# Kernel optimization log

Measured on AMD Instinct MI355X. Metric: run time of the kernel, lower is better.

The kernel has to match this reference:

```python
import jax, jax.numpy as jnp
import numpy as np

D_MODEL = 1024
N_HEADS = 16
D_HEAD = D_MODEL // N_HEADS  # 64
SCALE = 1.0 / float(np.sqrt(D_HEAD))


def setup_inputs() -> dict:
    key = jax.random.key(0)
    kx, kq, kk, kv, ko = jax.random.split(key, 5)
    B, L = 1, 4096
    x = jax.random.normal(kx, (B, L, D_MODEL), dtype=jnp.float32)
    init = 0.02  # small init so softmax isn't saturated
    Wq = jax.random.normal(kq, (D_MODEL, D_MODEL), dtype=jnp.float32) * init
    Wk = jax.random.normal(kk, (D_MODEL, D_MODEL), dtype=jnp.float32) * init
    Wv = jax.random.normal(kv, (D_MODEL, D_MODEL), dtype=jnp.float32) * init
    Wo = jax.random.normal(ko, (D_MODEL, D_MODEL), dtype=jnp.float32) * init
    return {"x": x, "Wq": Wq, "Wk": Wk, "Wv": Wv, "Wo": Wo}


def reference(x, Wq, Wk, Wv, Wo):
    # x: [B, L, d_model]; torch Linear (no bias): y = x @ W.T
    B, L, _ = x.shape

    def split_heads(t):  # [B, L, d_model] -> [B, H, L, Dh]
        return t.reshape(B, L, N_HEADS, D_HEAD).transpose(0, 2, 1, 3)

    q = split_heads(x @ Wq.T)
    k = split_heads(x @ Wk.T)
    v = split_heads(x @ Wv.T)

    # Full (non-flash) attention: explicit [B, H, L, L] scores (causal=False, eval dropout=0)
    scores = jnp.einsum("bhld,bhmd->bhlm", q, k) * SCALE
    attn = jax.nn.softmax(scores, axis=-1)
    out = jnp.einsum("bhlm,bhmd->bhld", attn, v)

    out = out.transpose(0, 2, 1, 3).reshape(B, L, D_MODEL)
    return out @ Wo.T
```

## Files before the change

### kernel.cpp

```cpp
#include <hip/hip_runtime.h>

typedef _Float16 f16_t;
typedef __fp16 fp16x2 __attribute__((ext_vector_type(2)));
typedef _Float16 f16x2 __attribute__((ext_vector_type(2)));
typedef _Float16 f16x4 __attribute__((ext_vector_type(4)));
typedef _Float16 f16x8 __attribute__((ext_vector_type(8)));
typedef float f32x4 __attribute__((ext_vector_type(4)));

#define D_MODEL 1024
#define LSEQ 4096
#define NH 16
#define DH 64
#define QSCALE 0.18033688011112042f

#define GLDS16(g, l)                                                     \
    __builtin_amdgcn_global_load_lds(                                    \
        (const __attribute__((address_space(1))) void*)(g),              \
        (__attribute__((address_space(3))) void*)(l), 16, 0, 0)

#define WAIT_VM(n) asm volatile("s_waitcnt vmcnt(" #n ")" ::: "memory")

__global__ __launch_bounds__(256) void cvt_x(const float* __restrict__ in,
                                             f16_t* __restrict__ out, int n) {
    int i = (blockIdx.x * 256 + threadIdx.x) * 4;
    if (i + 3 < n) {
        float4 v = *(const float4*)&in[i];
        alignas(8) f16_t o4[4] = {(f16_t)v.x, (f16_t)v.y, (f16_t)v.z, (f16_t)v.w};
        *(uint2*)&out[i] = *(const uint2*)o4;
    }
}

__global__ __launch_bounds__(256) void cvt_w4(const float* __restrict__ w0,
                                              const float* __restrict__ w1,
                                              const float* __restrict__ w2,
                                              const float* __restrict__ w3,
                                              f16_t* __restrict__ out) {
    const int q = blockIdx.y;
    const float* src = (q == 0) ? w0 : (q == 1) ? w1 : (q == 2) ? w2 : w3;
    const float scale = (q == 0) ? QSCALE : 1.f;
    int i = (blockIdx.x * 256 + threadIdx.x) * 4;
    float4 v = *(const float4*)&src[i];
    alignas(8) f16_t o4[4] = {(f16_t)(v.x * scale), (f16_t)(v.y * scale),
                              (f16_t)(v.z * scale), (f16_t)(v.w * scale)};
    *(uint2*)&out[(size_t)q * (D_MODEL * D_MODEL) + i] = *(const uint2*)o4;
}

__global__ __launch_bounds__(256, 3) void gemm_f16(const f16_t* __restrict__ A,
                                                   const f16_t* __restrict__ B,
                                                   void* __restrict__ Cout,
                                                   int M, int N, int K, int mode) {
    __shared__ alignas(16) f16_t As[3][128 * 32];
    __shared__ alignas(16) f16_t Bs[3][128 * 32];

    const int tid  = threadIdx.x;
    const int wave = tid >> 6;
    const int lane = tid & 63;
    const int quad = lane >> 4;
    const int l16  = lane & 15;
    const int wm = (wave & 1) * 64;
    const int wn = (wave >> 1) * 64;
    const int bm = blockIdx.x * 128;
    const int bn = blockIdx.y * 128;

    f32x4 acc[4][4] = {};
    const int nk = K / 32;

    auto stage = [&](int kt, int b) {
        const int c0 = wave * 2;
        GLDS16(&A[(size_t)(bm + c0 * 16 + l16) * K + kt * 32 + quad * 8],
               &As[b][c0 * 512]);
        GLDS16(&A[(size_t)(bm + (c0 + 1) * 16 + l16) * K + kt * 32 + quad * 8],
               &As[b][(c0 + 1) * 512]);
        GLDS16(&B[(size_t)(bn + c0 * 16 + l16) * K + kt * 32 + quad * 8],
               &Bs[b][c0 * 512]);
        GLDS16(&B[(size_t)(bn + (c0 + 1) * 16 + l16) * K + kt * 32 + quad * 8],
               &Bs[b][(c0 + 1) * 512]);
    };

    stage(0, 0);
    stage(1, 1);
    for (int kt = 0; kt < nk; ++kt) {
        const int cb = kt % 3;
        if (kt < nk - 1) WAIT_VM(4);
        else             WAIT_VM(0);
        __syncthreads();
        if (kt + 2 < nk) stage(kt + 2, (kt + 2) % 3);

        f16x8 af[4], bfr[4];
#pragma unroll
        for (int mt = 0; mt < 4; ++mt)
            af[mt] = *(const f16x8*)&As[cb][((wm >> 4) + mt) * 512 + lane * 8];
#pragma unroll
        for (int nt = 0; nt < 4; ++nt)
            bfr[nt] = *(const f16x8*)&Bs[cb][((wn >> 4) + nt) * 512 + lane * 8];
#pragma unroll
        for (int mt = 0; mt < 4; ++mt)
#pragma unroll
            for (int nt = 0; nt < 4; ++nt)
                acc[mt][nt] = __builtin_amdgcn_mfma_f32_16x16x32_f16(
                    bfr[nt], af[mt], acc[mt][nt], 0, 0, 0);
    }

#pragma unroll
    for (int mt = 0; mt < 4; ++mt)
#pragma unroll
        for (int nt = 0; nt < 4; ++nt) {
            int row = bm + wm + mt * 16 + l16;
            int col = bn + wn + nt * 16 + quad * 4;
            if (mode == 0) {
                f16x4 p = {(f16_t)acc[mt][nt][0], (f16_t)acc[mt][nt][1],
                           (f16_t)acc[mt][nt][2], (f16_t)acc[mt][nt][3]};
                *(f16x4*)&((f16_t*)Cout)[((size_t)(col >> 6) * M + row) * 64 +
                                         (col & 63)] = p;
            } else {
                *(f32x4*)&((float*)Cout)[(size_t)row * N + col] = acc[mt][nt];
            }
        }
}

__global__ __launch_bounds__(256) void transpose_v(const f16_t* __restrict__ vh,
                                                   f16_t* __restrict__ v4) {
    __shared__ f16_t Ts[64][72];
    const int t = threadIdx.x;
    const int lt = blockIdx.x;
    const int head = blockIdx.y;

#pragma unroll
    for (int i = 0; i < 2; ++i) {
        int idx = t + i * 256;
        int row = idx >> 3, part = idx & 7;
        *(uint4*)&Ts[row][part * 8] =
            *(const uint4*)&vh[((size_t)head * LSEQ + lt * 64 + row) * DH + part * 8];
    }
    __syncthreads();

    const int c   = t >> 4;
    const int dt  = c >> 2, kb = c & 3;
    const int km2 = (t & 15) >> 2;
    const int dl2 = t & 3;
    alignas(16) f16_t buf[16];
#pragma unroll
    for (int i = 0; i < 16; ++i) {
        int j = i & 3, dd = i >> 2;
        buf[i] = Ts[kb * 16 + km2 * 4 + j][dt * 16 + dl2 * 4 + dd];
    }
    f16_t* dst = v4 + (size_t)head * (LSEQ * DH) + lt * 4096 + c * 256 + (t & 15) * 16;
    *(uint4*)&dst[0] = *(const uint4*)&buf[0];
    *(uint4*)&dst[8] = *(const uint4*)&buf[8];
}

__global__ __launch_bounds__(512, 2) void attn_kernel(const f16_t* __restrict__ qh,
                                                      const f16_t* __restrict__ kh,
                                                      const f16_t* __restrict__ v4,
                                                      f16_t* __restrict__ ao) {
    __shared__ alignas(16) f16_t smem[32768];
    __shared__ alignas(16) float lscr[16 * 64];
    f16_t* KsB = smem;
    f16_t* VsB = smem + 16384;

    const int tid  = threadIdx.x;
    const int wave = tid >> 6;
    const int lane = tid & 63;
    const int quad = lane >> 4;
    const int l16  = lane & 15;
    const int wq   = wave & 3;
    const int kha  = wave >> 2;

    const int id = blockIdx.x;
    const int head = id & 15;
    const int qrow0 = (id >> 4) * 256 + wq * 64;

    const f16_t* Q  = qh + (size_t)head * LSEQ * DH;
    const f16_t* K  = kh + (size_t)head * LSEQ * DH;
    const f16_t* V4 = v4 + (size_t)head * (LSEQ * DH);

    f16x8 qf[4][2];
#pragma unroll
    for (int qt = 0; qt < 4; ++qt)
#pragma unroll
        for (int kc = 0; kc < 2; ++kc)
            qf[qt][kc] = *(const f16x8*)
                &Q[(size_t)(qrow0 + qt * 16 + l16) * DH + kc * 32 + quad * 8];

    f32x4 o[4][4] = {};
    float lp[4] = {0.f, 0.f, 0.f, 0.f};

    auto stage = [&](int kt, int b) {
        f16_t* ks = KsB + (kha * 2 + b) * 4096;
        f16_t* vs = VsB + (kha * 2 + b) * 4096;
        const int ktg = kha * 32 + kt;
#pragma unroll
        for (int jj = 0; jj < 2; ++jj) {
            const int j = wq * 2 + jj;
            GLDS16(&K[(size_t)(ktg * 64 + wq * 16 + l16) * DH + jj * 32 + quad * 8],
                   &ks[j * 512]);
            GLDS16(&V4[(size_t)ktg * 4096 + wq * 1024 + jj * 512 + lane * 8],
                   &vs[wq * 1024 + jj * 512]);
        }
    };

    const int NT = LSEQ / 2 / 64;
    stage(0, 0);
    for (int kt = 0; kt < NT; ++kt) {
        const int cb = kt & 1;
        WAIT_VM(0);
        __syncthreads();
        if (kt + 1 < NT) stage(kt + 1, cb ^ 1);

        const f16_t* ks = KsB + (kha * 2 + cb) * 4096;
        const f16_t* vs = VsB + (kha * 2 + cb) * 4096;

#pragma unroll
        for (int mt = 0; mt < 4; ++mt) {
            f16x8 kf0 = *(const f16x8*)&ks[(mt * 2 + 0) * 512 + lane * 8];
            f16x8 kf1 = *(const f16x8*)&ks[(mt * 2 + 1) * 512 + lane * 8];

            f32x4 s[4] = {};
#pragma unroll
            for (int qt = 0; qt < 4; ++qt) {
                s[qt] = __builtin_amdgcn_mfma_f32_16x16x32_f16(kf0, qf[qt][0],
                                                               s[qt], 0, 0, 0);
                s[qt] = __builtin_amdgcn_mfma_f32_16x16x32_f16(kf1, qf[qt][1],
                                                               s[qt], 0, 0, 0);
            }

            f16x4 vfd[4];
#pragma unroll
            for (int dt = 0; dt < 4; ++dt)
                vfd[dt] = *(const f16x4*)&vs[(dt * 4 + mt) * 256 + lane * 4];

#pragma unroll
            for (int qt = 0; qt < 4; ++qt) {
                float e0 = __builtin_amdgcn_exp2f(s[qt][0]);
                float e1 = __builtin_amdgcn_exp2f(s[qt][1]);
                float e2 = __builtin_amdgcn_exp2f(s[qt][2]);
                float e3 = __builtin_amdgcn_exp2f(s[qt][3]);
                lp[qt] += (e0 + e1) + (e2 + e3);
                fp16x2 p01 = __builtin_amdgcn_cvt_pkrtz(e0, e1);
                fp16x2 p23 = __builtin_amdgcn_cvt_pkrtz(e2, e3);
                f16x4 p = {__builtin_bit_cast(f16x2, p01)[0],
                           __builtin_bit_cast(f16x2, p01)[1],
                           __builtin_bit_cast(f16x2, p23)[0],
                           __builtin_bit_cast(f16x2, p23)[1]};
#pragma unroll
                for (int dt = 0; dt < 4; ++dt)
                    o[dt][qt] = __builtin_amdgcn_mfma_f32_16x16x16f16(
                        vfd[dt], p, o[dt][qt], 0, 0, 0);
            }
        }
    }

    __syncthreads();
    float* scr = (float*)smem;
    if (wave >= 4) {
#pragma unroll
        for (int dt = 0; dt < 4; ++dt)
#pragma unroll
            for (int qt = 0; qt < 4; ++qt)
                *(f32x4*)&scr[(((wave - 4) * 16 + dt * 4 + qt) * 64 + lane) * 4] =
                    o[dt][qt];
#pragma unroll
        for (int qt = 0; qt < 4; ++qt)
            lscr[((wave - 4) * 4 + qt) * 64 + lane] = lp[qt];
    }
    __syncthreads();
    if (wave < 4) {
#pragma unroll
        for (int dt = 0; dt < 4; ++dt)
#pragma unroll
            for (int qt = 0; qt < 4; ++qt)
                o[dt][qt] += *(const f32x4*)
                    &scr[((wave * 16 + dt * 4 + qt) * 64 + lane) * 4];
#pragma unroll
        for (int qt = 0; qt < 4; ++qt) {
            float t = lp[qt] + lscr[(wave * 4 + qt) * 64 + lane];
            t += __shfl_xor(t, 16, 64);
            t += __shfl_xor(t, 32, 64);
            lp[qt] = 1.f / t;
        }
#pragma unroll
        for (int dt = 0; dt < 4; ++dt)
#pragma unroll
            for (int qt = 0; qt < 4; ++qt) {
                f16x4 ov = {(f16_t)(o[dt][qt][0] * lp[qt]),
                            (f16_t)(o[dt][qt][1] * lp[qt]),
                            (f16_t)(o[dt][qt][2] * lp[qt]),
                            (f16_t)(o[dt][qt][3] * lp[qt])};
                int qrow = qrow0 + qt * 16 + l16;
                *(f16x4*)&ao[(size_t)qrow * D_MODEL + head * 64 + dt * 16 +
                             quad * 4] = ov;
            }
    }
}

extern "C" void kernel_launch(void* const* d_in, const int* in_sizes, int n_in,
                              void* d_out, int out_size, void* d_ws, size_t ws_size,
                              hipStream_t stream) {
    const float* x  = (const float*)d_in[0];
    const float* Wq = (const float*)d_in[1];
    const float* Wk = (const float*)d_in[2];
    const float* Wv = (const float*)d_in[3];
    const float* Wo = (const float*)d_in[4];

    f16_t* xb = (f16_t*)d_ws;
    f16_t* wq = xb + (size_t)LSEQ * D_MODEL;
    f16_t* wo = wq + (size_t)3 * D_MODEL * D_MODEL;
    f16_t* qh = wo + (size_t)D_MODEL * D_MODEL;
    f16_t* kh = qh + (size_t)LSEQ * D_MODEL;
    f16_t* vh = kh + (size_t)LSEQ * D_MODEL;
    f16_t* v4 = vh + (size_t)LSEQ * D_MODEL;
    f16_t* ao = v4 + (size_t)LSEQ * D_MODEL;

    const int nx = LSEQ * D_MODEL;
    cvt_x<<<nx / 1024, 256, 0, stream>>>(x, xb, nx);
    cvt_w4<<<dim3(D_MODEL * D_MODEL / 1024, 4), 256, 0, stream>>>(Wq, Wk, Wv, Wo, wq);

    gemm_f16<<<dim3(LSEQ / 128, 3 * D_MODEL / 128), 256, 0, stream>>>(
        xb, wq, qh, LSEQ, 3 * D_MODEL, D_MODEL, 0);

    transpose_v<<<dim3(LSEQ / 64, NH), 256, 0, stream>>>(vh, v4);

    attn_kernel<<<dim3((LSEQ / 256) * NH), 512, 0, stream>>>(qh, kh, v4, ao);

    gemm_f16<<<dim3(LSEQ / 128, D_MODEL / 128), 256, 0, stream>>>(
        ao, wo, d_out, LSEQ, D_MODEL, D_MODEL, 1);
}
```

Measured before the change: 259.9 us.

## Use 16x16x32 MFMA for PV product with re-laid-out V tiles

The PV accumulation now pairs two 16-key score tiles and issues a single 16x16x32 f16 MFMA per output tile instead of two 16x16x16 MFMAs. To feed it, the V transpose kernel is rewritten so each lane's 8-element fragment holds keys from two 16-key subtiles in the order the packed probabilities use. Halving the PV MFMA count and using wider LDS reads should raise matrix-core throughput. In exchange it keeps more score registers live, which may affect occupancy at 2 blocks per CU.

New measurement: 249.7 us. 1.04x faster.

```diff
diff --git a/kernel.cpp b/kernel.cpp
--- a/kernel.cpp
+++ b/kernel.cpp
@@ -134,17 +134,21 @@
     }
     __syncthreads();
 
-    const int c   = t >> 4;
-    const int dt  = c >> 2, kb = c & 3;
-    const int km2 = (t & 15) >> 2;
-    const int dl2 = t & 3;
+    const int c8  = t >> 5;
+    const int mtp = c8 >> 2, dt = c8 & 3;
+    const int l0  = (t & 31) * 2;
     alignas(16) f16_t buf[16];
 #pragma unroll
-    for (int i = 0; i < 16; ++i) {
-        int j = i & 3, dd = i >> 2;
-        buf[i] = Ts[kb * 16 + km2 * 4 + j][dt * 16 + dl2 * 4 + dd];
-    }
-    f16_t* dst = v4 + (size_t)head * (LSEQ * DH) + lt * 4096 + c * 256 + (t & 15) * 16;
+    for (int li = 0; li < 2; ++li) {
+        const int l = l0 + li;
+        const int g = l >> 4, l16 = l & 15;
+#pragma unroll
+        for (int j = 0; j < 8; ++j) {
+            int key = mtp * 32 + (j < 4 ? 4 * g + j : 16 + 4 * g + (j - 4));
+            buf[li * 8 + j] = Ts[key][dt * 16 + l16];
+        }
+    }
+    f16_t* dst = v4 + (size_t)head * (LSEQ * DH) + (size_t)lt * 4096 + c8 * 512 + l0 * 8;
     *(uint4*)&dst[0] = *(const uint4*)&buf[0];
     *(uint4*)&dst[8] = *(const uint4*)&buf[8];
 }
@@ -211,40 +215,53 @@
         const f16_t* vs = VsB + (kha * 2 + cb) * 4096;
 
 #pragma unroll
-        for (int mt = 0; mt < 4; ++mt) {
-            f16x8 kf0 = *(const f16x8*)&ks[(mt * 2 + 0) * 512 + lane * 8];
-            f16x8 kf1 = *(const f16x8*)&ks[(mt * 2 + 1) * 512 + lane * 8];
-
-            f32x4 s[4] = {};
+        for (int mtp = 0; mtp < 2; ++mtp) {
+            f32x4 s[2][4] = {};
+#pragma unroll
+            for (int h = 0; h < 2; ++h) {
+                const int mt = mtp * 2 + h;
+                f16x8 kf0 = *(const f16x8*)&ks[(mt * 2 + 0) * 512 + lane * 8];
+                f16x8 kf1 = *(const f16x8*)&ks[(mt * 2 + 1) * 512 + lane * 8];
+#pragma unroll
+                for (int qt = 0; qt < 4; ++qt) {
+                    s[h][qt] = __builtin_amdgcn_mfma_f32_16x16x32_f16(
+                        kf0, qf[qt][0], s[h][qt], 0, 0, 0);
+                    s[h][qt] = __builtin_amdgcn_mfma_f32_16x16x32_f16(
+                        kf1, qf[qt][1], s[h][qt], 0, 0, 0);
+                }
+            }
+
+            f16x8 vfd[4];
+#pragma unroll
+            for (int dt = 0; dt < 4; ++dt)
+                vfd[dt] = *(const f16x8*)&vs[(mtp * 4 + dt) * 512 + lane * 8];
+
 #pragma unroll
             for (int qt = 0; qt < 4; ++qt) {
-                s[qt] = __builtin_amdgcn_mfma_f32_16x16x32_f16(kf0, qf[qt][0],
-                                                               s[qt], 0, 0, 0);
-                s[qt] = __builtin_amdgcn_mfma_f32_16x16x32_f16(kf1, qf[qt][1],
-                                                               s[qt], 0, 0, 0);
-            }
-
-            f16x4 vfd[4];
-#pragma unroll
-            for (int dt = 0; dt < 4; ++dt)
-                vfd[dt] = *(const f16x4*)&vs[(dt * 4 + mt) * 256 + lane * 4];
-
-#pragma unroll
-            for (int qt = 0; qt < 4; ++qt) {
-                float e0 = __builtin_amdgcn_exp2f(s[qt][0]);
-                float e1 = __builtin_amdgcn_exp2f(s[qt][1]);
-                float e2 = __builtin_amdgcn_exp2f(s[qt][2]);
-                float e3 = __builtin_amdgcn_exp2f(s[qt][3]);
-                lp[qt] += (e0 + e1) + (e2 + e3);
+                float e0 = __builtin_amdgcn_exp2f(s[0][qt][0]);
+                float e1 = __builtin_amdgcn_exp2f(s[0][qt][1]);
+                float e2 = __builtin_amdgcn_exp2f(s[0][qt][2]);
+                float e3 = __builtin_amdgcn_exp2f(s[0][qt][3]);
+                float e4 = __builtin_amdgcn_exp2f(s[1][qt][0]);
+                float e5 = __builtin_amdgcn_exp2f(s[1][qt][1]);
+                float e6 = __builtin_amdgcn_exp2f(s[1][qt][2]);
+                float e7 = __builtin_amdgcn_exp2f(s[1][qt][3]);
+                lp[qt] += ((e0 + e1) + (e2 + e3)) + ((e4 + e5) + (e6 + e7));
                 fp16x2 p01 = __builtin_amdgcn_cvt_pkrtz(e0, e1);
                 fp16x2 p23 = __builtin_amdgcn_cvt_pkrtz(e2, e3);
-                f16x4 p = {__builtin_bit_cast(f16x2, p01)[0],
+                fp16x2 p45 = __builtin_amdgcn_cvt_pkrtz(e4, e5);
+                fp16x2 p67 = __builtin_amdgcn_cvt_pkrtz(e6, e7);
+                f16x8 p = {__builtin_bit_cast(f16x2, p01)[0],
                            __builtin_bit_cast(f16x2, p01)[1],
                            __builtin_bit_cast(f16x2, p23)[0],
-                           __builtin_bit_cast(f16x2, p23)[1]};
+                           __builtin_bit_cast(f16x2, p23)[1],
+                           __builtin_bit_cast(f16x2, p45)[0],
+                           __builtin_bit_cast(f16x2, p45)[1],
+                           __builtin_bit_cast(f16x2, p67)[0],
+                           __builtin_bit_cast(f16x2, p67)[1]};
 #pragma unroll
                 for (int dt = 0; dt < 4; ++dt)
-                    o[dt][qt] = __builtin_amdgcn_mfma_f32_16x16x16f16(
+                    o[dt][qt] = __builtin_amdgcn_mfma_f32_16x16x32_f16(
                         vfd[dt], p, o[dt][qt], 0, 0, 0);
             }
         }
```
